# Kernel tuning notes

Hardware: AMD Instinct MI355X
Metric: run time of the kernel (lower is better)

Reference implementation:

```python
import jax, jax.numpy as jnp
import numpy as np

EPS = 1e-5

def sage_layer(x, src, dst, n_tgt, Wl, bl, Wr, gamma, beta):
    # mean aggregation of source features over incoming edges per target
    msg = x[src]                                         # [E, C] irregular gather
    s = jax.ops.segment_sum(msg, dst, num_segments=n_tgt)
    cnt = jax.ops.segment_sum(jnp.ones((src.shape[0],), x.dtype), dst, num_segments=n_tgt)
    aggr = s / jnp.maximum(cnt, 1.0)[:, None]
    x_tgt = x[:n_tgt]
    h = aggr @ Wl.T + bl + x_tgt @ Wr.T                  # SAGEConv: lin_l(aggr)+lin_r(root)
    h = jax.nn.relu(h)
    mu = jnp.mean(h, axis=0)
    var = jnp.mean((h - mu) ** 2, axis=0)                # biased var (torch BN training)
    return gamma * (h - mu) * jax.lax.rsqrt(var + EPS) + beta

def setup_inputs() -> dict:
    key = jax.random.key(0)
    ks = jax.random.split(key, 16)
    C = 256
    N0, N1, N2 = 200000, 50000, 12500
    E0, E1 = 800000, 400000
    sc = 1.0 / np.sqrt(C)
    return {
        "x": jax.random.normal(ks[0], (N0, C), jnp.float32),
        "ei0_src": jax.random.randint(ks[1], (E0,), 0, N0),
        "ei0_dst": jax.random.randint(ks[2], (E0,), 0, N1),
        "ei1_src": jax.random.randint(ks[3], (E1,), 0, N1),
        "ei1_dst": jax.random.randint(ks[4], (E1,), 0, N2),
        "Wl0": jax.random.normal(ks[5], (C, C), jnp.float32) * sc,
        "bl0": jnp.zeros((C,), jnp.float32),
        "Wr0": jax.random.normal(ks[6], (C, C), jnp.float32) * sc,
        "g0": jnp.ones((C,), jnp.float32),
        "be0": jnp.zeros((C,), jnp.float32),
        "Wl1": jax.random.normal(ks[7], (C, C), jnp.float32) * sc,
        "bl1": jnp.zeros((C,), jnp.float32),
        "Wr1": jax.random.normal(ks[8], (C, C), jnp.float32) * sc,
        "g1": jnp.ones((C,), jnp.float32),
        "be1": jnp.zeros((C,), jnp.float32),
    }

def reference(x, ei0_src, ei0_dst, ei1_src, ei1_dst,
              Wl0, bl0, Wr0, g0, be0, Wl1, bl1, Wr1, g1, be1):
    N1, N2 = 50000, 12500
    x = sage_layer(x, ei0_src, ei0_dst, N1, Wl0, bl0, Wr0, g0, be0)
    x = sage_layer(x, ei1_src, ei1_dst, N2, Wl1, bl1, Wr1, g1, be1)
    return x
```

## Files before the change

kernel.cpp:

```cpp
#include <hip/hip_runtime.h>
#include <cstddef>
#include <cstdint>

#define C 256

typedef __attribute__((ext_vector_type(8))) short short8;
typedef __attribute__((ext_vector_type(4))) float f32x4;

__device__ __forceinline__ ushort f2bf(float f) {
    uint32_t u = __float_as_uint(f);
    u += 0x7FFF + ((u >> 16) & 1);
    return (ushort)(u >> 16);
}
__device__ __forceinline__ float bf2f(ushort u) {
    return __uint_as_float(((uint32_t)u) << 16);
}
__device__ __forceinline__ uint2 pack4(float a, float b, float c, float d) {
    uint2 o;
    o.x = (uint32_t)f2bf(a) | ((uint32_t)f2bf(b) << 16);
    o.y = (uint32_t)f2bf(c) | ((uint32_t)f2bf(d) << 16);
    return o;
}
__device__ __forceinline__ uint4 pack8(float4 a, float4 b) {
    uint4 o;
    o.x = (uint32_t)f2bf(a.x) | ((uint32_t)f2bf(a.y) << 16);
    o.y = (uint32_t)f2bf(a.z) | ((uint32_t)f2bf(a.w) << 16);
    o.z = (uint32_t)f2bf(b.x) | ((uint32_t)f2bf(b.y) << 16);
    o.w = (uint32_t)f2bf(b.z) | ((uint32_t)f2bf(b.w) << 16);
    return o;
}
__device__ __forceinline__ void acc8(uint4 v, float* a) {
    a[0] += bf2f((ushort)(v.x & 0xffff)); a[1] += bf2f((ushort)(v.x >> 16));
    a[2] += bf2f((ushort)(v.y & 0xffff)); a[3] += bf2f((ushort)(v.y >> 16));
    a[4] += bf2f((ushort)(v.z & 0xffff)); a[5] += bf2f((ushort)(v.z >> 16));
    a[6] += bf2f((ushort)(v.w & 0xffff)); a[7] += bf2f((ushort)(v.w >> 16));
}

#define PB_CAST 6400
#define PB_W    64
#define PB_H0   1024
#define PB_H1   512

__global__ __launch_bounds__(256) void prep_kernel(
        const float4* __restrict__ x4, int nx8, uint4* __restrict__ xbf4,
        const float4* __restrict__ wl0f, const float4* __restrict__ wr0f,
        uint4* __restrict__ wl0b, uint4* __restrict__ wr0b,
        const int* __restrict__ e0d, int* __restrict__ cnt0, int E0,
        const int* __restrict__ e1d, int* __restrict__ cnt1, int E1) {
    const int b = blockIdx.x;
    if (b < PB_CAST) {
        const int stride = PB_CAST * 256;
        for (int i = b * 256 + threadIdx.x; i < nx8; i += stride) {
            float4 lo = x4[2 * (size_t)i];
            float4 hi = x4[2 * (size_t)i + 1];
            xbf4[i] = pack8(lo, hi);
        }
    } else if (b < PB_CAST + PB_W) {
        const int nw8 = C * C / 8;
        const int stride = PB_W * 256;
        for (int i = (b - PB_CAST) * 256 + threadIdx.x; i < 2 * nw8; i += stride) {
            if (i < nw8) {
                float4 lo = wl0f[2 * i], hi = wl0f[2 * i + 1];
                wl0b[i] = pack8(lo, hi);
            } else {
                int j = i - nw8;
                float4 lo = wr0f[2 * j], hi = wr0f[2 * j + 1];
                wr0b[j] = pack8(lo, hi);
            }
        }
    } else if (b < PB_CAST + PB_W + PB_H0) {
        const int stride = PB_H0 * 256;
        for (int i = (b - PB_CAST - PB_W) * 256 + threadIdx.x; i < E0; i += stride)
            atomicAdd(&cnt0[e0d[i]], 1);
    } else {
        const int stride = PB_H1 * 256;
        for (int i = (b - PB_CAST - PB_W - PB_H0) * 256 + threadIdx.x; i < E1; i += stride)
            atomicAdd(&cnt1[e1d[i]], 1);
    }
}

__global__ __launch_bounds__(1024) void scan2_kernel(
        const int* __restrict__ cnt0, int* __restrict__ off0, int n0,
        const int* __restrict__ cnt1, int* __restrict__ off1, int n1) {
    const int* cnt = blockIdx.x ? cnt1 : cnt0;
    int* off = blockIdx.x ? off1 : off0;
    int n = blockIdx.x ? n1 : n0;
    __shared__ int buf[1024];
    int chunk = (n + 1023) >> 10;
    int lo = (int)threadIdx.x * chunk;
    int hi = min(lo + chunk, n);
    int s = 0;
    for (int i = lo; i < hi; ++i) s += cnt[i];
    buf[threadIdx.x] = s;
    __syncthreads();
    int xv = s;
    for (int d = 1; d < 1024; d <<= 1) {
        int t = ((int)threadIdx.x >= d) ? buf[threadIdx.x - d] : 0;
        __syncthreads();
        xv += t;
        buf[threadIdx.x] = xv;
        __syncthreads();
    }
    int run = xv - s;
    for (int i = lo; i < hi; ++i) { off[i] = run; run += cnt[i]; }
    if (lo < n && hi == n) off[n] = run;
}

__global__ void scatter2_kernel(
        const int* __restrict__ s0, const int* __restrict__ d0,
        const int* __restrict__ off0, int* __restrict__ cnt0, int* __restrict__ esrc0, int E0,
        const int* __restrict__ s1, const int* __restrict__ d1,
        const int* __restrict__ off1, int* __restrict__ cnt1, int* __restrict__ esrc1, int E1) {
    int e = blockIdx.x * blockDim.x + threadIdx.x;
    if (e < E0) {
        int d = d0[e];
        int old = atomicSub(&cnt0[d], 1);
        esrc0[off0[d] + old - 1] = s0[e];
    } else if (e < E0 + E1) {
        int i = e - E0;
        int d = d1[i];
        int old = atomicSub(&cnt1[d], 1);
        esrc1[off1[d] + old - 1] = s1[i];
    }
}

__global__ __launch_bounds__(256) void aggregate_kernel(const uint4* __restrict__ xb4,
        const int* __restrict__ esrc, const int* __restrict__ off,
        uint4* __restrict__ out4, int n_tgt) {
    const int lane = threadIdx.x & 63;
    const int half = lane >> 5, l31 = lane & 31;
    const int t = blockIdx.x * 4 + (threadIdx.x >> 6);
    if (t >= n_tgt) return;
    const int base = off[t];
    const int deg = off[t + 1] - base;
    float a[8] = {0.f, 0.f, 0.f, 0.f, 0.f, 0.f, 0.f, 0.f};
    int i = 0;
    for (; i + 4 <= deg; i += 4) {
        int s0 = esrc[base + i + half];
        int s1 = esrc[base + i + 2 + half];
        uint4 v0 = xb4[(size_t)s0 * 32 + l31];
        uint4 v1 = xb4[(size_t)s1 * 32 + l31];
        acc8(v0, a);
        acc8(v1, a);
    }
    for (; i + 2 <= deg; i += 2) {
        int s = esrc[base + i + half];
        uint4 v = xb4[(size_t)s * 32 + l31];
        acc8(v, a);
    }
    if ((deg & 1) && half == 0) {
        int s = esrc[base + deg - 1];
        uint4 v = xb4[(size_t)s * 32 + l31];
        acc8(v, a);
    }
#pragma unroll
    for (int j = 0; j < 8; ++j) a[j] += __shfl_xor(a[j], 32, 64);
    if (half == 0) {
        float inv = 1.0f / (float)(deg > 1 ? deg : 1);
        uint4 o;
        o.x = (uint32_t)f2bf(a[0] * inv) | ((uint32_t)f2bf(a[1] * inv) << 16);
        o.y = (uint32_t)f2bf(a[2] * inv) | ((uint32_t)f2bf(a[3] * inv) << 16);
        o.z = (uint32_t)f2bf(a[4] * inv) | ((uint32_t)f2bf(a[5] * inv) << 16);
        o.w = (uint32_t)f2bf(a[6] * inv) | ((uint32_t)f2bf(a[7] * inv) << 16);
        out4[(size_t)t * 32 + l31] = o;
    }
}

__global__ __launch_bounds__(256) void aggregate_f32_kernel(const float4* __restrict__ x4,
        const int* __restrict__ esrc, const int* __restrict__ off,
        uint2* __restrict__ aggr, int n_tgt) {
    int w = threadIdx.x >> 6;
    int lane = threadIdx.x & 63;
    int t = blockIdx.x * 4 + w;
    if (t >= n_tgt) return;
    int base = off[t];
    int deg = off[t + 1] - base;
    float4 acc = make_float4(0.f, 0.f, 0.f, 0.f);
    for (int i = 0; i < deg; ++i) {
        int s = esrc[base + i];
        float4 v = x4[(size_t)s * 64 + lane];
        acc.x += v.x; acc.y += v.y; acc.z += v.z; acc.w += v.w;
    }
    float inv = 1.0f / (float)(deg > 1 ? deg : 1);
    aggr[(size_t)t * 64 + lane] = pack4(acc.x * inv, acc.y * inv, acc.z * inv, acc.w * inv);
}

#define TM 128
#define TN 128
#define LDK 40

__global__ __launch_bounds__(256) void gemm_bn_mfma(
        const ushort* __restrict__ Aagg, const ushort* __restrict__ Axt,
        const ushort* __restrict__ Wl,  const ushort* __restrict__ Wr,
        const float* __restrict__ bias,
        ushort* __restrict__ h, float* __restrict__ colsum, float* __restrict__ colsq,
        int M) {
    __shared__ ushort As[TM * LDK];
    __shared__ ushort Bs[TN * LDK];
    __shared__ float csum[TN];
    __shared__ float csq[TN];

    const int tid = threadIdx.x;
    const int m0 = blockIdx.y * TM;
    const int n0 = blockIdx.x * TN;
    const int wid = tid >> 6, lane = tid & 63;
    const int l15 = lane & 15, quad = lane >> 4;
    const int wm = (wid & 1) * 64, wn = (wid >> 1) * 64;

    if (tid < TN) { csum[tid] = 0.f; csq[tid] = 0.f; }

    const int srow = tid >> 2;
    const int skoff = (tid & 3) * 8;

    f32x4 acc[4][4];
#pragma unroll
    for (int i = 0; i < 4; ++i)
#pragma unroll
        for (int j = 0; j < 4; ++j) acc[i][j] = (f32x4){0.f, 0.f, 0.f, 0.f};

#pragma unroll 1
    for (int kt = 0; kt < 16; ++kt) {
        const int ks = kt * 32;
        const ushort* Ab = (ks < 256) ? Aagg : Axt;
        const ushort* Bb = (ks < 256) ? Wl : Wr;
        const int k0 = ks & 255;
        int r0 = min(m0 + srow, M - 1);
        int r1 = min(m0 + srow + 64, M - 1);
        uint4 a0 = *(const uint4*)&Ab[(size_t)r0 * C + k0 + skoff];
        uint4 a1 = *(const uint4*)&Ab[(size_t)r1 * C + k0 + skoff];
        uint4 b0 = *(const uint4*)&Bb[(size_t)(n0 + srow) * C + k0 + skoff];
        uint4 b1 = *(const uint4*)&Bb[(size_t)(n0 + srow + 64) * C + k0 + skoff];
        __syncthreads();
        *(uint4*)&As[srow * LDK + skoff] = a0;
        *(uint4*)&As[(srow + 64) * LDK + skoff] = a1;
        *(uint4*)&Bs[srow * LDK + skoff] = b0;
        *(uint4*)&Bs[(srow + 64) * LDK + skoff] = b1;
        __syncthreads();

        short8 af[4], bw[4];
#pragma unroll
        for (int mi = 0; mi < 4; ++mi)
            af[mi] = *(const short8*)&As[(wm + mi * 16 + l15) * LDK + quad * 8];
#pragma unroll
        for (int ni = 0; ni < 4; ++ni)
            bw[ni] = *(const short8*)&Bs[(wn + ni * 16 + l15) * LDK + quad * 8];
#pragma unroll
        for (int mi = 0; mi < 4; ++mi)
#pragma unroll
            for (int ni = 0; ni < 4; ++ni)
                acc[mi][ni] = __builtin_amdgcn_mfma_f32_16x16x32_bf16(
                    af[mi], bw[ni], acc[mi][ni], 0, 0, 0);
    }

    float lsum[4] = {0.f, 0.f, 0.f, 0.f};
    float lsq[4]  = {0.f, 0.f, 0.f, 0.f};
#pragma unroll
    for (int ni = 0; ni < 4; ++ni) {
        const int col = wn + ni * 16 + l15;
        const float bv = bias[n0 + col];
#pragma unroll
        for (int mi = 0; mi < 4; ++mi) {
#pragma unroll
            for (int r = 0; r < 4; ++r) {
                int m = m0 + wm + mi * 16 + quad * 4 + r;
                float v = acc[mi][ni][r] + bv;
                v = fmaxf(v, 0.f);
                if (m < M) {
                    h[(size_t)m * C + n0 + col] = f2bf(v);
                    lsum[ni] += v;
                    lsq[ni] += v * v;
                }
            }
        }
    }
#pragma unroll
    for (int ni = 0; ni < 4; ++ni) {
        const int col = wn + ni * 16 + l15;
        atomicAdd(&csum[col], lsum[ni]);
        atomicAdd(&csq[col], lsq[ni]);
    }
    __syncthreads();
    if (tid < TN) {
        atomicAdd(&colsum[n0 + tid], csum[tid]);
        atomicAdd(&colsq[n0 + tid], csq[tid]);
    }
}

__global__ __launch_bounds__(256) void fixup_kernel(
        const float* __restrict__ colsum, const float* __restrict__ colsq, float invN,
        const float* __restrict__ g0, const float* __restrict__ be0,
        const float* __restrict__ Wl1, const float* __restrict__ Wr1,
        const float* __restrict__ bl1,
        ushort* __restrict__ wl1b, ushort* __restrict__ wr1b, float* __restrict__ bias1) {
    __shared__ float ss[C], st[C];
    __shared__ float red[256];
    const int k = threadIdx.x;
    {
        float m = colsum[k] * invN;
        float v = colsq[k] * invN - m * m;
        float r = rsqrtf(fmaxf(v, 0.f) + 1e-5f);
        float s = g0[k] * r;
        ss[k] = s;
        st[k] = be0[k] - m * s;
    }
    __syncthreads();
    const int n = blockIdx.x;
    float wl = Wl1[(size_t)n * C + k];
    float wr = Wr1[(size_t)n * C + k];
    wl1b[(size_t)n * C + k] = f2bf(wl * ss[k]);
    wr1b[(size_t)n * C + k] = f2bf(wr * ss[k]);
    red[k] = st[k] * (wl + wr);
    __syncthreads();
    for (int d = 128; d > 0; d >>= 1) {
        if (k < d) red[k] += red[k + d];
        __syncthreads();
    }
    if (k == 0) bias1[n] = bl1[n] + red[0];
}

__global__ __launch_bounds__(256) void norm1_kernel(const uint2* __restrict__ hin,
        const float* __restrict__ colsum, const float* __restrict__ colsq, float invN,
        const float* __restrict__ gamma, const float* __restrict__ beta,
        float4* __restrict__ outp, int n4) {
    __shared__ float smu[C], srs[C];
    {
        int k = threadIdx.x;
        float m = colsum[k] * invN;
        float v = colsq[k] * invN - m * m;
        smu[k] = m;
        srs[k] = rsqrtf(fmaxf(v, 0.f) + 1e-5f);
    }
    __syncthreads();
    int i = blockIdx.x * blockDim.x + threadIdx.x;
    if (i >= n4) return;
    int c = (i & 63) << 2;
    uint2 v = hin[i];
    float4 o;
    o.x = gamma[c + 0] * (bf2f((ushort)(v.x & 0xffff)) - smu[c + 0]) * srs[c + 0] + beta[c + 0];
    o.y = gamma[c + 1] * (bf2f((ushort)(v.x >> 16))    - smu[c + 1]) * srs[c + 1] + beta[c + 1];
    o.z = gamma[c + 2] * (bf2f((ushort)(v.y & 0xffff)) - smu[c + 2]) * srs[c + 2] + beta[c + 2];
    o.w = gamma[c + 3] * (bf2f((ushort)(v.y >> 16))    - smu[c + 3]) * srs[c + 3] + beta[c + 3];
    outp[i] = o;
}

extern "C" void kernel_launch(void* const* d_in, const int* in_sizes, int n_in,
                              void* d_out, int out_size, void* d_ws, size_t ws_size,
                              hipStream_t stream) {
    const float* x   = (const float*)d_in[0];
    const int* e0s   = (const int*)d_in[1];
    const int* e0d   = (const int*)d_in[2];
    const int* e1s   = (const int*)d_in[3];
    const int* e1d   = (const int*)d_in[4];
    const float* Wl0 = (const float*)d_in[5];
    const float* bl0 = (const float*)d_in[6];
    const float* Wr0 = (const float*)d_in[7];
    const float* ga0 = (const float*)d_in[8];
    const float* be0 = (const float*)d_in[9];
    const float* Wl1 = (const float*)d_in[10];
    const float* bl1 = (const float*)d_in[11];
    const float* Wr1 = (const float*)d_in[12];
    const float* ga1 = (const float*)d_in[13];
    const float* be1 = (const float*)d_in[14];

    const int N0 = 200000, N1 = 50000, N2 = 12500;
    const int E0 = in_sizes[1];
    const int E1 = in_sizes[3];

    char* ws = (char*)d_ws;
    size_t o = 0;
    auto alloc = [&](size_t bytes) -> char* {
        char* p = ws + o;
        o += (bytes + 255) & ~(size_t)255;
        return p;
    };

    const size_t common =
        (size_t)N1 * C * 2 * 2 + (size_t)E0 * 4 + (size_t)E1 * 4 +
        ((size_t)N1 + N2 + 8 * C) * 4 + ((size_t)N1 + N2 + 2) * 4 +
        4 * (size_t)C * C * 2 + C * 4 + 65536;
    const bool full = ws_size >= common + (size_t)N0 * C * 2;

    int* cnt0 = (int*)alloc(((size_t)N1 + N2 + 8 * C) * sizeof(int));
    int* cnt1 = cnt0 + N1;
    float* stats = (float*)(cnt1 + N2);
    float* colsum0 = stats,         *colsq0 = stats + C;
    float* colsum1 = stats + 4 * C, *colsq1 = stats + 5 * C;
    const size_t zbytes = ((size_t)N1 + N2 + 8 * C) * sizeof(int);

    int* off0 = (int*)alloc(((size_t)N1 + 1) * sizeof(int));
    int* off1 = (int*)alloc(((size_t)N2 + 1) * sizeof(int));
    ushort* x_bf  = (ushort*)alloc((full ? (size_t)N0 : (size_t)N1) * C * 2);
    ushort* aggr0 = (ushort*)alloc((size_t)N1 * C * 2);
    ushort* h0raw = (ushort*)alloc((size_t)N1 * C * 2);
    ushort* aggr1 = aggr0;
    ushort* h1raw = aggr0 + (size_t)N2 * C;
    int* esrc0 = (int*)alloc((size_t)E0 * sizeof(int));
    int* esrc1 = (int*)alloc((size_t)E1 * sizeof(int));
    ushort* wbf = (ushort*)alloc(4 * (size_t)C * C * 2);
    ushort* wl0b = wbf, *wr0b = wbf + C * C, *wl1b = wbf + 2 * C * C, *wr1b = wbf + 3 * C * C;
    float* bias1 = (float*)alloc(C * sizeof(float));

    hipMemsetAsync(cnt0, 0, zbytes, stream);

    {
        int nx8 = (full ? N0 : N1) * C / 8;
        prep_kernel<<<PB_CAST + PB_W + PB_H0 + PB_H1, 256, 0, stream>>>(
            (const float4*)x, nx8, (uint4*)x_bf,
            (const float4*)Wl0, (const float4*)Wr0, (uint4*)wl0b, (uint4*)wr0b,
            e0d, cnt0, E0, e1d, cnt1, E1);
    }
    scan2_kernel<<<2, 1024, 0, stream>>>(cnt0, off0, N1, cnt1, off1, N2);
    scatter2_kernel<<<(E0 + E1 + 255) / 256, 256, 0, stream>>>(
        e0s, e0d, off0, cnt0, esrc0, E0, e1s, e1d, off1, cnt1, esrc1, E1);

    if (full)
        aggregate_kernel<<<N1 / 4, 256, 0, stream>>>((const uint4*)x_bf, esrc0, off0,
                                                     (uint4*)aggr0, N1);
    else
        aggregate_f32_kernel<<<N1 / 4, 256, 0, stream>>>((const float4*)x, esrc0, off0,
                                                         (uint2*)aggr0, N1);
    dim3 grid0(C / TN, (N1 + TM - 1) / TM);
    gemm_bn_mfma<<<grid0, 256, 0, stream>>>(aggr0, x_bf, wl0b, wr0b, bl0,
                                            h0raw, colsum0, colsq0, N1);
    fixup_kernel<<<C, 256, 0, stream>>>(colsum0, colsq0, 1.0f / (float)N1,
                                        ga0, be0, Wl1, Wr1, bl1, wl1b, wr1b, bias1);

    aggregate_kernel<<<N2 / 4, 256, 0, stream>>>((const uint4*)h0raw, esrc1, off1,
                                                 (uint4*)aggr1, N2);
    dim3 grid1(C / TN, (N2 + TM - 1) / TM);
    gemm_bn_mfma<<<grid1, 256, 0, stream>>>(aggr1, h0raw, wl1b, wr1b, bias1,
                                            h1raw, colsum1, colsq1, N2);
    int n4_1 = N2 * C / 4;
    norm1_kernel<<<(n4_1 + 255) / 256, 256, 0, stream>>>((const uint2*)h1raw,
                                                         colsum1, colsq1, 1.0f / (float)N2,
                                                         ga1, be1, (float4*)d_out, n4_1);
}
```

Baseline: 686.1 us.

## Split prep into cast and histogram kernels, deepen aggregate gather unroll

```diff
diff --git a/kernel.cpp b/kernel.cpp
--- a/kernel.cpp
+++ b/kernel.cpp
@@ -21,14 +21,6 @@
     o.y = (uint32_t)f2bf(c) | ((uint32_t)f2bf(d) << 16);
     return o;
 }
-__device__ __forceinline__ uint4 pack8(float4 a, float4 b) {
-    uint4 o;
-    o.x = (uint32_t)f2bf(a.x) | ((uint32_t)f2bf(a.y) << 16);
-    o.y = (uint32_t)f2bf(a.z) | ((uint32_t)f2bf(a.w) << 16);
-    o.z = (uint32_t)f2bf(b.x) | ((uint32_t)f2bf(b.y) << 16);
-    o.w = (uint32_t)f2bf(b.z) | ((uint32_t)f2bf(b.w) << 16);
-    return o;
-}
 __device__ __forceinline__ void acc8(uint4 v, float* a) {
     a[0] += bf2f((ushort)(v.x & 0xffff)); a[1] += bf2f((ushort)(v.x >> 16));
     a[2] += bf2f((ushort)(v.y & 0xffff)); a[3] += bf2f((ushort)(v.y >> 16));
@@ -36,45 +28,42 @@
     a[6] += bf2f((ushort)(v.w & 0xffff)); a[7] += bf2f((ushort)(v.w >> 16));
 }
 
-#define PB_CAST 6400
-#define PB_W    64
-#define PB_H0   1024
-#define PB_H1   512
-
-__global__ __launch_bounds__(256) void prep_kernel(
-        const float4* __restrict__ x4, int nx8, uint4* __restrict__ xbf4,
+__global__ __launch_bounds__(256) void cast_kernel(
+        const float4* __restrict__ x4, int nx4, uint2* __restrict__ xbf,
         const float4* __restrict__ wl0f, const float4* __restrict__ wr0f,
-        uint4* __restrict__ wl0b, uint4* __restrict__ wr0b,
+        uint2* __restrict__ wl0b, uint2* __restrict__ wr0b) {
+    const int nw4 = C * C / 4;
+    const int total = nx4 + 2 * nw4;
+    const int stride = gridDim.x * blockDim.x;
+    for (int i = blockIdx.x * blockDim.x + threadIdx.x; i < total; i += stride) {
+        if (i < nx4) {
+            float4 v = x4[i];
+            xbf[i] = pack4(v.x, v.y, v.z, v.w);
+        } else if (i < nx4 + nw4) {
+            int j = i - nx4;
+            float4 v = wl0f[j];
+            wl0b[j] = pack4(v.x, v.y, v.z, v.w);
+        } else {
+            int j = i - nx4 - nw4;
+            float4 v = wr0f[j];
+            wr0b[j] = pack4(v.x, v.y, v.z, v.w);
+        }
+    }
+}
+
+#define HB0 2048
+#define HB1 1024
+__global__ __launch_bounds__(256) void hist_kernel(
         const int* __restrict__ e0d, int* __restrict__ cnt0, int E0,
         const int* __restrict__ e1d, int* __restrict__ cnt1, int E1) {
     const int b = blockIdx.x;
-    if (b < PB_CAST) {
-        const int stride = PB_CAST * 256;
-        for (int i = b * 256 + threadIdx.x; i < nx8; i += stride) {
-            float4 lo = x4[2 * (size_t)i];
-            float4 hi = x4[2 * (size_t)i + 1];
-            xbf4[i] = pack8(lo, hi);
-        }
-    } else if (b < PB_CAST + PB_W) {
-        const int nw8 = C * C / 8;
-        const int stride = PB_W * 256;
-        for (int i = (b - PB_CAST) * 256 + threadIdx.x; i < 2 * nw8; i += stride) {
-            if (i < nw8) {
-                float4 lo = wl0f[2 * i], hi = wl0f[2 * i + 1];
-                wl0b[i] = pack8(lo, hi);
-            } else {
-                int j = i - nw8;
-                float4 lo = wr0f[2 * j], hi = wr0f[2 * j + 1];
-                wr0b[j] = pack8(lo, hi);
-            }
-        }
-    } else if (b < PB_CAST + PB_W + PB_H0) {
-        const int stride = PB_H0 * 256;
-        for (int i = (b - PB_CAST - PB_W) * 256 + threadIdx.x; i < E0; i += stride)
+    if (b < HB0) {
+        const int stride = HB0 * 256;
+        for (int i = b * 256 + threadIdx.x; i < E0; i += stride)
             atomicAdd(&cnt0[e0d[i]], 1);
     } else {
-        const int stride = PB_H1 * 256;
-        for (int i = (b - PB_CAST - PB_W - PB_H0) * 256 + threadIdx.x; i < E1; i += stride)
+        const int stride = HB1 * 256;
+        for (int i = (b - HB0) * 256 + threadIdx.x; i < E1; i += stride)
             atomicAdd(&cnt1[e1d[i]], 1);
     }
 }
@@ -135,13 +124,16 @@
     const int deg = off[t + 1] - base;
     float a[8] = {0.f, 0.f, 0.f, 0.f, 0.f, 0.f, 0.f, 0.f};
     int i = 0;
-    for (; i + 4 <= deg; i += 4) {
+    for (; i + 8 <= deg; i += 8) {
         int s0 = esrc[base + i + half];
         int s1 = esrc[base + i + 2 + half];
+        int s2 = esrc[base + i + 4 + half];
+        int s3 = esrc[base + i + 6 + half];
         uint4 v0 = xb4[(size_t)s0 * 32 + l31];
         uint4 v1 = xb4[(size_t)s1 * 32 + l31];
-        acc8(v0, a);
-        acc8(v1, a);
+        uint4 v2 = xb4[(size_t)s2 * 32 + l31];
+        uint4 v3 = xb4[(size_t)s3 * 32 + l31];
+        acc8(v0, a); acc8(v1, a); acc8(v2, a); acc8(v3, a);
     }
     for (; i + 2 <= deg; i += 2) {
         int s = esrc[base + i + half];
@@ -403,12 +395,12 @@
     hipMemsetAsync(cnt0, 0, zbytes, stream);
 
     {
-        int nx8 = (full ? N0 : N1) * C / 8;
-        prep_kernel<<<PB_CAST + PB_W + PB_H0 + PB_H1, 256, 0, stream>>>(
-            (const float4*)x, nx8, (uint4*)x_bf,
-            (const float4*)Wl0, (const float4*)Wr0, (uint4*)wl0b, (uint4*)wr0b,
-            e0d, cnt0, E0, e1d, cnt1, E1);
-    }
+        int nx4 = (full ? N0 : N1) * C / 4;
+        cast_kernel<<<6400, 256, 0, stream>>>((const float4*)x, nx4, (uint2*)x_bf,
+                                              (const float4*)Wl0, (const float4*)Wr0,
+                                              (uint2*)wl0b, (uint2*)wr0b);
+    }
+    hist_kernel<<<HB0 + HB1, 256, 0, stream>>>(e0d, cnt0, E0, e1d, cnt1, E1);
     scan2_kernel<<<2, 1024, 0, stream>>>(cnt0, off0, N1, cnt1, off1, N2);
     scatter2_kernel<<<(E0 + E1 + 255) / 256, 256, 0, stream>>>(
         e0s, e0d, off0, cnt0, esrc0, E0, e1s, e1d, off1, cnt1, esrc1, E1);
```

New measurement: 697.6 us. No clear change (+1.7%).
